# Performance work log

Measured on AMD Instinct MI355X. Metric: run time of the kernel, lower is better.

Reference implementation:

```python
import jax, jax.numpy as jnp
import numpy as np


def setup_inputs() -> dict:
    key = jax.random.key(0)
    ks = jax.random.split(key, 12)
    B, C, H, W = 8, 256, 64, 64
    C8 = C // 8
    s = lambda *sh: 0.02
    inp = {
        "x1": jax.random.normal(ks[0], (B, C, H, W), jnp.float32),
        "x2": jax.random.normal(ks[1], (B, C, H, W), jnp.float32),
        # DFEM.conv1 (1x1), shared for x1 and x2
        "w1": jax.random.normal(ks[2], (C, C), jnp.float32) * 0.02,
        "b1": jax.random.normal(ks[3], (C,), jnp.float32) * 0.02,
        # PAM projections (1x1 convs)
        "wq": jax.random.normal(ks[4], (C8, C), jnp.float32) * 0.02,
        "bq": jax.random.normal(ks[5], (C8,), jnp.float32) * 0.02,
        "wk": jax.random.normal(ks[6], (C8, C), jnp.float32) * 0.02,
        "bk": jax.random.normal(ks[7], (C8,), jnp.float32) * 0.02,
        "wv": jax.random.normal(ks[8], (C, C), jnp.float32) * 0.02,
        "bv": jax.random.normal(ks[9], (C,), jnp.float32) * 0.02,
        # gamma initialized to zero in the original; use small nonzero so PAM path matters
        "gamma": jnp.full((1,), 0.5, jnp.float32),
        # SpatialAttention 3x3 conv, 2->1 channels, no bias (OIHW)
        "w_sa": jax.random.normal(ks[10], (1, 2, 3, 3), jnp.float32) * 0.1,
    }
    return inp


def _conv1x1(x, w, b):
    # x: [B,C,H,W], w: [O,C], b: [O]
    return jnp.einsum("oc,bchw->bohw", w, x) + b[None, :, None, None]


def _pam(x, wq, bq, wk, bk, wv, bv, gamma):
    B, C, H, W = x.shape
    N = H * W
    xf = x.reshape(B, C, N)
    q = jnp.einsum("oc,bcn->bon", wq, xf) + bq[None, :, None]  # [B,C/8,N]
    k = jnp.einsum("oc,bcn->bon", wk, xf) + bk[None, :, None]  # [B,C/8,N]
    v = jnp.einsum("oc,bcn->bon", wv, xf) + bv[None, :, None]  # [B,C,N]
    energy = jnp.einsum("bci,bcj->bij", q, k)                  # [B,N,N] (no scaling, as in source)
    att = jax.nn.softmax(energy, axis=-1)
    out = jnp.einsum("bcj,bij->bci", v, att).reshape(B, C, H, W)
    return gamma[0] * out + x


def _spatial_attention(x, w_sa):
    # x: [B,2C,H,W] -> [B,1,H,W]
    avg_out = jnp.mean(x, axis=1, keepdims=True)
    max_out = jnp.max(x, axis=1, keepdims=True)
    cat = jnp.concatenate([avg_out, max_out], axis=1)  # [B,2,H,W]
    y = jax.lax.conv_general_dilated(
        cat, w_sa, window_strides=(1, 1), padding=((1, 1), (1, 1)),
        dimension_numbers=("NCHW", "OIHW", "NCHW"))
    return jax.nn.sigmoid(y)


def reference(x1, x2, w1, b1, wq, bq, wk, bk, wv, bv, gamma, w_sa):
    x11 = _conv1x1(x1, w1, b1)
    x21 = _conv1x1(x2, w1, b1)
    weight = _spatial_attention(jnp.concatenate([x11, x21], axis=1), w_sa)
    out1 = _pam(x11, wq, bq, wk, bk, wv, bv, gamma)
    out2 = _pam(x21, wq, bq, wk, bk, wv, bv, gamma)
    a = x1 * out1
    b = x2 * out2
    return weight * jnp.abs(b - a)
```

## Files before the change

### kernel.cpp

```cpp
#include <hip/hip_runtime.h>
#include <stdint.h>

#define B_ 8
#define C_ 256
#define N_ 4096
#define C8_ 32
#define LOG2E 1.4426950408889634f

typedef __attribute__((ext_vector_type(8))) short s16x8;
typedef __attribute__((ext_vector_type(4))) float f32x4;

static __device__ __forceinline__ unsigned short f2bf(float f) {
  union { float f; unsigned u; } v; v.f = f;
  unsigned r = v.u + 0x7FFFu + ((v.u >> 16) & 1u);
  return (unsigned short)(r >> 16);
}
static __device__ __forceinline__ float bf2f(unsigned short h) {
  union { unsigned u; float f; } v; v.u = ((unsigned)h) << 16;
  return v.f;
}
static __device__ __forceinline__ unsigned cvtpk(float lo, float hi) {
  unsigned r;
  asm("v_cvt_pk_bf16_f32 %0, %1, %2" : "=v"(r) : "v"(lo), "v"(hi));
  return r;
}

#define OFS_X1T  0ull
#define OFS_X2T  16777216ull
#define OFS_X11T 33554432ull
#define OFS_X21T 50331648ull
#define OFS_Q1   67108864ull
#define OFS_K1   69206016ull
#define OFS_Q2   71303168ull
#define OFS_K2   73400320ull
#define OFS_V1   75497472ull
#define OFS_V2   92274688ull
#define OFS_OA1  OFS_X1T
#define OFS_OA2  OFS_X2T
#define OFS_MM   109051904ull
#define OFS_WGT  109314048ull
#define OFS_W1B  109445120ull
#define OFS_WQB  109576192ull
#define OFS_WKB  109592576ull
#define OFS_WVB  109608960ull

__global__ __launch_bounds__(256) void k_transpose(
    const float* __restrict__ x1, const float* __restrict__ x2,
    unsigned short* __restrict__ x1t, unsigned short* __restrict__ x2t) {
  __shared__ unsigned short lds[64 * 66];
  const int t = threadIdx.x;
  const int b = blockIdx.z >> 1, s = blockIdx.z & 1;
  const float* src = s ? x2 : x1;
  unsigned short* dst = s ? x2t : x1t;
  const int n0 = blockIdx.x * 64, c0 = blockIdx.y * 64;
  const int nl = t & 63;
#pragma unroll
  for (int r = 0; r < 16; ++r) {
    const int cl = (t >> 6) + 4 * r;
    lds[nl * 66 + cl] = f2bf(src[((size_t)(b * C_ + c0 + cl)) * N_ + n0 + nl]);
  }
  __syncthreads();
  const int c2 = t & 31;
#pragma unroll
  for (int r = 0; r < 8; ++r) {
    const int n = (t >> 5) + 8 * r;
    const unsigned uv = *(const unsigned*)(&lds[n * 66 + 2 * c2]);
    *(unsigned*)(&dst[((size_t)(b * N_ + n0 + n)) * C_ + c0 + 2 * c2]) = uv;
  }
}

__global__ __launch_bounds__(256) void k_wconv(
    const float* __restrict__ w1, const float* __restrict__ wq,
    const float* __restrict__ wk, const float* __restrict__ wv,
    unsigned short* __restrict__ w1b, unsigned short* __restrict__ wqb,
    unsigned short* __restrict__ wkb, unsigned short* __restrict__ wvb) {
  const int i = blockIdx.x * 256 + threadIdx.x;
  if (i < 65536) { w1b[i] = f2bf(w1[i]); wvb[i] = f2bf(wv[i]); }
  if (i < 8192)  { wqb[i] = f2bf(wq[i]); wkb[i] = f2bf(wk[i]); }
}

__global__ __launch_bounds__(256) void k_conv(
    const unsigned short* __restrict__ X1, const unsigned short* __restrict__ X2,
    const unsigned short* __restrict__ W, const float* __restrict__ bias,
    unsigned short* __restrict__ O1, unsigned short* __restrict__ O2) {
  const unsigned short* X = blockIdx.z ? X2 : X1;
  unsigned short* OUT = blockIdx.z ? O2 : O1;
  const int b = blockIdx.y;
  const int lane = threadIdx.x & 63, wave = threadIdx.x >> 6;
  const int li = lane & 15, g = lane >> 4;
  const int nbase = blockIdx.x * 64 + wave * 16;
  const f32x4 zero4 = {0.f, 0.f, 0.f, 0.f};
  f32x4 acc[16];
#pragma unroll
  for (int f = 0; f < 16; ++f) acc[f] = zero4;
  const unsigned short* xrow = X + ((size_t)b * N_ + nbase + li) * C_ + 8 * g;
#pragma unroll
  for (int kk = 0; kk < 8; ++kk) {
    const s16x8 a = *(const s16x8*)(xrow + kk * 32);
#pragma unroll
    for (int f = 0; f < 16; ++f) {
      const s16x8 wf = *(const s16x8*)(W + ((size_t)(f * 16 + li)) * C_ + kk * 32 + 8 * g);
      acc[f] = __builtin_amdgcn_mfma_f32_16x16x32_bf16(wf, a, acc[f], 0, 0, 0);
    }
  }
  unsigned short* orow = OUT + ((size_t)b * N_ + nbase + li) * C_ + 4 * g;
#pragma unroll
  for (int f = 0; f < 16; ++f) {
    const float4 bb = *(const float4*)(bias + f * 16 + 4 * g);
    const unsigned lo = cvtpk(acc[f][0] + bb.x, acc[f][1] + bb.y);
    const unsigned hi = cvtpk(acc[f][2] + bb.z, acc[f][3] + bb.w);
    *(uint2*)(orow + f * 16) = make_uint2(lo, hi);
  }
}

__global__ __launch_bounds__(256) void k_qk(
    const unsigned short* __restrict__ X1, const unsigned short* __restrict__ X2,
    const unsigned short* __restrict__ WQ, const unsigned short* __restrict__ WK,
    const float* __restrict__ bq, const float* __restrict__ bk,
    unsigned short* __restrict__ Q1o, unsigned short* __restrict__ Q2o,
    unsigned short* __restrict__ K1o, unsigned short* __restrict__ K2o) {
  const unsigned short* X = blockIdx.z ? X2 : X1;
  unsigned short* Qo = blockIdx.z ? Q2o : Q1o;
  unsigned short* Ko = blockIdx.z ? K2o : K1o;
  const int b = blockIdx.y;
  const int lane = threadIdx.x & 63, wave = threadIdx.x >> 6;
  const int li = lane & 15, g = lane >> 4;
  const int nbase = blockIdx.x * 64 + wave * 16;
  const f32x4 zero4 = {0.f, 0.f, 0.f, 0.f};
  f32x4 aq[2], ak[2];
#pragma unroll
  for (int f = 0; f < 2; ++f) { aq[f] = zero4; ak[f] = zero4; }
  const unsigned short* xrow = X + ((size_t)b * N_ + nbase + li) * C_ + 8 * g;
#pragma unroll
  for (int kk = 0; kk < 8; ++kk) {
    const s16x8 a = *(const s16x8*)(xrow + kk * 32);
#pragma unroll
    for (int f = 0; f < 2; ++f) {
      const s16x8 wqf = *(const s16x8*)(WQ + ((size_t)(f * 16 + li)) * C_ + kk * 32 + 8 * g);
      const s16x8 wkf = *(const s16x8*)(WK + ((size_t)(f * 16 + li)) * C_ + kk * 32 + 8 * g);
      aq[f] = __builtin_amdgcn_mfma_f32_16x16x32_bf16(wqf, a, aq[f], 0, 0, 0);
      ak[f] = __builtin_amdgcn_mfma_f32_16x16x32_bf16(wkf, a, ak[f], 0, 0, 0);
    }
  }
  unsigned short* qrow = Qo + ((size_t)b * N_ + nbase + li) * C8_ + 4 * g;
  unsigned short* krow = Ko + ((size_t)b * N_ + nbase + li) * C8_ + 4 * g;
#pragma unroll
  for (int f = 0; f < 2; ++f) {
    const float4 bbq = *(const float4*)(bq + f * 16 + 4 * g);
    const float4 bbk = *(const float4*)(bk + f * 16 + 4 * g);
    const unsigned qlo = cvtpk((aq[f][0] + bbq.x) * LOG2E, (aq[f][1] + bbq.y) * LOG2E);
    const unsigned qhi = cvtpk((aq[f][2] + bbq.z) * LOG2E, (aq[f][3] + bbq.w) * LOG2E);
    const unsigned klo = cvtpk(ak[f][0] + bbk.x, ak[f][1] + bbk.y);
    const unsigned khi = cvtpk(ak[f][2] + bbk.z, ak[f][3] + bbk.w);
    *(uint2*)(qrow + f * 16) = make_uint2(qlo, qhi);
    *(uint2*)(krow + f * 16) = make_uint2(klo, khi);
  }
}

__global__ __launch_bounds__(256) void k_gemm_v(
    const unsigned short* __restrict__ X1, const unsigned short* __restrict__ X2,
    const unsigned short* __restrict__ W, const float* __restrict__ bias,
    unsigned short* __restrict__ V1o, unsigned short* __restrict__ V2o) {
  const int b = blockIdx.z >> 1, s = blockIdx.z & 1;
  const unsigned short* X = s ? X2 : X1;
  unsigned short* OUT = s ? V2o : V1o;
  const int lane = threadIdx.x & 63, wave = threadIdx.x >> 6;
  const int li = lane & 15, g = lane >> 4;
  const int obase = blockIdx.x * 64 + wave * 16;
  const int nbase = blockIdx.y * 256;
  const f32x4 zero4 = {0.f, 0.f, 0.f, 0.f};
  f32x4 acc[16];
#pragma unroll
  for (int f = 0; f < 16; ++f) acc[f] = zero4;
  const unsigned short* wrow = W + ((size_t)(obase + li)) * C_ + 8 * g;
#pragma unroll
  for (int kk = 0; kk < 8; ++kk) {
    const s16x8 a = *(const s16x8*)(wrow + kk * 32);
#pragma unroll
    for (int fn = 0; fn < 16; ++fn) {
      const s16x8 xf = *(const s16x8*)(X + ((size_t)b * N_ + nbase + fn * 16 + li) * C_ + kk * 32 + 8 * g);
      acc[fn] = __builtin_amdgcn_mfma_f32_16x16x32_bf16(xf, a, acc[fn], 0, 0, 0);
    }
  }
  const float bb = bias[obase + li];
  unsigned short* orow = OUT + ((size_t)b * C_ + obase + li) * N_ + nbase + 4 * g;
#pragma unroll
  for (int fn = 0; fn < 16; ++fn) {
    const unsigned lo = cvtpk(acc[fn][0] + bb, acc[fn][1] + bb);
    const unsigned hi = cvtpk(acc[fn][2] + bb, acc[fn][3] + bb);
    *(uint2*)(orow + fn * 16) = make_uint2(lo, hi);
  }
}

__global__ __launch_bounds__(256, 2) void k_flash2(
    const unsigned short* __restrict__ Q1, const unsigned short* __restrict__ K1,
    const unsigned short* __restrict__ V1, unsigned short* __restrict__ OA1,
    const unsigned short* __restrict__ Q2, const unsigned short* __restrict__ K2,
    const unsigned short* __restrict__ V2, unsigned short* __restrict__ OA2) {
  __shared__ __attribute__((aligned(16))) unsigned short vtile[2][8192];
  __shared__ __attribute__((aligned(16))) unsigned short ptile[4][1024];
  const int t = threadIdx.x;
  int f = blockIdx.x;
  f = (f & 7) * 64 + (f >> 3);
  const int z = f >> 5, qt = f & 31;
  const int b = z >> 1, src = z & 1;
  const unsigned short* Qp = src ? Q2 : Q1;
  const unsigned short* Kp = src ? K2 : K1;
  const unsigned short* Vp = src ? V2 : V1;
  unsigned short* OAp = (src ? OA2 : OA1) + (size_t)b * C_ * N_;

  const int lane = t & 63, wave = t >> 6;
  const int li = lane & 15, g = lane >> 4;
  const int rsw = (li >> 1) & 3;
  const f32x4 zero4 = {0.f, 0.f, 0.f, 0.f};

  const unsigned short* Vb = Vp + (size_t)b * C_ * N_;
  const unsigned short* Kb = Kp + (size_t)b * N_ * C8_;
  const int qbase = qt * 128 + wave * 32;

  s16x8 qf[2];
#pragma unroll
  for (int ib = 0; ib < 2; ++ib)
    qf[ib] = *(const s16x8*)(Qp + ((size_t)b * N_ + qbase + ib * 16 + li) * C8_ + 8 * g);

  f32x4 acc[2][16];
#pragma unroll
  for (int ib = 0; ib < 2; ++ib)
#pragma unroll
    for (int fc = 0; fc < 16; ++fc) acc[ib][fc] = zero4;
  float lsum[2] = {0.f, 0.f};

  const int vrow0 = t >> 2, vJ = t & 3;
  const int vwoff = ((vJ ^ ((vrow0 >> 1) & 3)) << 4);
  const int prd = ((g ^ rsw) << 4);
  const int psw0 = (((g >> 1) ^ rsw) << 4) + (g & 1) * 8;
  const int psw1 = ((((g >> 1) | 2) ^ rsw) << 4) + (g & 1) * 8;
  char* const pb = (char*)ptile[wave];

  int4 vreg[4];
#pragma unroll
  for (int rep = 0; rep < 4; ++rep)
    vreg[rep] = *(const int4*)(Vb + (size_t)(vrow0 + rep * 64) * N_ + vJ * 8);
  s16x8 kf0, kf1;
  {
    const unsigned short* kp = Kb + (size_t)li * C8_ + 8 * g;
    kf0 = *(const s16x8*)kp;
    kf1 = *(const s16x8*)(kp + 16 * C8_);
  }
#pragma unroll
  for (int rep = 0; rep < 4; ++rep)
    *(int4*)((char*)vtile[0] + (vrow0 + rep * 64) * 64 + vwoff) = vreg[rep];
  __syncthreads();

  for (int jt = 0; jt < 128; ++jt) {
    const int cur = jt & 1;
    const int jbn = ((jt + 1) & 127) * 32;
#pragma unroll
    for (int rep = 0; rep < 4; ++rep)
      vreg[rep] = *(const int4*)(Vb + (size_t)(vrow0 + rep * 64) * N_ + jbn + vJ * 8);
    s16x8 kn0, kn1;
    {
      const unsigned short* kp = Kb + (size_t)(jbn + li) * C8_ + 8 * g;
      kn0 = *(const s16x8*)kp;
      kn1 = *(const s16x8*)(kp + 16 * C8_);
    }

#pragma unroll
    for (int ib = 0; ib < 2; ++ib) {
      const f32x4 s0 = __builtin_amdgcn_mfma_f32_16x16x32_bf16(kf0, qf[ib], zero4, 0, 0, 0);
      const f32x4 s1 = __builtin_amdgcn_mfma_f32_16x16x32_bf16(kf1, qf[ib], zero4, 0, 0, 0);
      const float p0 = exp2f(s0[0] - 8.f), p1 = exp2f(s0[1] - 8.f);
      const float p2 = exp2f(s0[2] - 8.f), p3 = exp2f(s0[3] - 8.f);
      const float p4 = exp2f(s1[0] - 8.f), p5 = exp2f(s1[1] - 8.f);
      const float p6 = exp2f(s1[2] - 8.f), p7 = exp2f(s1[3] - 8.f);
      lsum[ib] += ((p0 + p1) + (p2 + p3)) + ((p4 + p5) + (p6 + p7));
      const unsigned u01 = cvtpk(p0, p1), u23 = cvtpk(p2, p3);
      const unsigned u45 = cvtpk(p4, p5), u67 = cvtpk(p6, p7);
      char* const pr = pb + (ib * 16 + li) * 64;
      *(uint2*)(pr + psw0) = make_uint2(u01, u23);
      *(uint2*)(pr + psw1) = make_uint2(u45, u67);
    }

    const s16x8 pb0 = *(const s16x8*)(pb + li * 64 + prd);
    const s16x8 pb1 = *(const s16x8*)(pb + (16 + li) * 64 + prd);
    char* const vt = (char*)vtile[cur];
#pragma unroll
    for (int fc = 0; fc < 16; ++fc) {
      const s16x8 vf = *(const s16x8*)(vt + (fc * 16 + li) * 64 + prd);
      acc[0][fc] = __builtin_amdgcn_mfma_f32_16x16x32_bf16(vf, pb0, acc[0][fc], 0, 0, 0);
      acc[1][fc] = __builtin_amdgcn_mfma_f32_16x16x32_bf16(vf, pb1, acc[1][fc], 0, 0, 0);
    }

#pragma unroll
    for (int rep = 0; rep < 4; ++rep)
      *(int4*)((char*)vtile[cur ^ 1] + (vrow0 + rep * 64) * 64 + vwoff) = vreg[rep];
    kf0 = kn0; kf1 = kn1;
    __syncthreads();
  }

#pragma unroll
  for (int ib = 0; ib < 2; ++ib) {
    float ls = lsum[ib];
    ls += __shfl_xor(ls, 16);
    ls += __shfl_xor(ls, 32);
    const float inv = 1.0f / ls;
    unsigned short* oab = OAp + qbase + ib * 16 + li;
#pragma unroll
    for (int fc = 0; fc < 16; ++fc) {
#pragma unroll
      for (int r = 0; r < 4; ++r) {
        oab[(size_t)(fc * 16 + 4 * g + r) * N_] = f2bf(acc[ib][fc][r] * inv);
      }
    }
  }
}

__global__ __launch_bounds__(256) void k_sared(
    const unsigned short* __restrict__ x11t, const unsigned short* __restrict__ x21t,
    float* __restrict__ mm) {
  const int row = blockIdx.x * 4 + (threadIdx.x >> 6);
  const int lane = threadIdx.x & 63;
  float s = 0.f, mx = -1e30f;
  const uint2 a = *(const uint2*)(x11t + (size_t)row * C_ + lane * 4);
  const uint2 c = *(const uint2*)(x21t + (size_t)row * C_ + lane * 4);
  const unsigned vals[4] = {a.x, a.y, c.x, c.y};
#pragma unroll
  for (int k = 0; k < 4; ++k) {
    const float f0 = bf2f((unsigned short)(vals[k] & 0xffff));
    const float f1 = bf2f((unsigned short)(vals[k] >> 16));
    s += f0 + f1;
    mx = fmaxf(mx, fmaxf(f0, f1));
  }
#pragma unroll
  for (int off = 1; off < 64; off <<= 1) {
    s += __shfl_xor(s, off);
    mx = fmaxf(mx, __shfl_xor(mx, off));
  }
  if (lane == 0) {
    const int b = row >> 12, n = row & 4095;
    mm[(size_t)b * 8192 + n] = s * (1.f / 512.f);
    mm[(size_t)b * 8192 + 4096 + n] = mx;
  }
}

__global__ __launch_bounds__(256) void k_saconv(
    const float* __restrict__ mm, const float* __restrict__ wsa, float* __restrict__ wgt) {
  const int gi = blockIdx.x * 256 + threadIdx.x;
  const int b = gi >> 12, n = gi & 4095, h = n >> 6, w = n & 63;
  float acc = 0.f;
#pragma unroll
  for (int ky = 0; ky < 3; ++ky) {
#pragma unroll
    for (int kx = 0; kx < 3; ++kx) {
      const int hh = h + ky - 1, ww = w + kx - 1;
      if (hh >= 0 && hh < 64 && ww >= 0 && ww < 64) {
        const int nn = hh * 64 + ww;
        acc += mm[(size_t)b * 8192 + nn] * wsa[ky * 3 + kx];
        acc += mm[(size_t)b * 8192 + 4096 + nn] * wsa[9 + ky * 3 + kx];
      }
    }
  }
  wgt[gi] = 1.f / (1.f + __expf(-acc));
}

__global__ __launch_bounds__(256) void k_final(
    const float* __restrict__ x1, const float* __restrict__ x2,
    const unsigned short* __restrict__ x11t, const unsigned short* __restrict__ x21t,
    const unsigned short* __restrict__ oa1, const unsigned short* __restrict__ oa2,
    const float* __restrict__ wgt, const float* __restrict__ gamma,
    float* __restrict__ out) {
  __shared__ unsigned short t1[64 * 66], t2[64 * 66];
  const int t = threadIdx.x;
  const int b = blockIdx.z, c0 = blockIdx.y * 64, n0 = blockIdx.x * 64;
#pragma unroll
  for (int r = 0; r < 16; ++r) {
    const int nl = (t >> 6) + 4 * r, cl = t & 63;
    const size_t idx = ((size_t)b * N_ + n0 + nl) * C_ + c0 + cl;
    t1[nl * 66 + cl] = x11t[idx];
    t2[nl * 66 + cl] = x21t[idx];
  }
  __syncthreads();
  const float gam = gamma[0];
#pragma unroll
  for (int r = 0; r < 16; ++r) {
    const int cl = (t >> 6) + 4 * r, nl = t & 63;
    const size_t idx = ((size_t)b * C_ + c0 + cl) * N_ + n0 + nl;
    const float o1 = gam * bf2f(oa1[idx]) + bf2f(t1[nl * 66 + cl]);
    const float o2 = gam * bf2f(oa2[idx]) + bf2f(t2[nl * 66 + cl]);
    const float av = x1[idx] * o1;
    const float bv = x2[idx] * o2;
    out[idx] = wgt[(size_t)b * N_ + n0 + nl] * fabsf(bv - av);
  }
}

extern "C" void kernel_launch(void* const* d_in, const int* in_sizes, int n_in,
                              void* d_out, int out_size, void* d_ws, size_t ws_size,
                              hipStream_t stream) {
  const float* x1 = (const float*)d_in[0];
  const float* x2 = (const float*)d_in[1];
  const float* w1 = (const float*)d_in[2];
  const float* b1 = (const float*)d_in[3];
  const float* wq = (const float*)d_in[4];
  const float* bq = (const float*)d_in[5];
  const float* wk = (const float*)d_in[6];
  const float* bk = (const float*)d_in[7];
  const float* wv = (const float*)d_in[8];
  const float* bv = (const float*)d_in[9];
  const float* gamma = (const float*)d_in[10];
  const float* wsa = (const float*)d_in[11];
  float* out = (float*)d_out;
  char* ws = (char*)d_ws;

  unsigned short* x1T  = (unsigned short*)(ws + OFS_X1T);
  unsigned short* x2T  = (unsigned short*)(ws + OFS_X2T);
  unsigned short* x11T = (unsigned short*)(ws + OFS_X11T);
  unsigned short* x21T = (unsigned short*)(ws + OFS_X21T);
  unsigned short* Q1   = (unsigned short*)(ws + OFS_Q1);
  unsigned short* K1   = (unsigned short*)(ws + OFS_K1);
  unsigned short* Q2   = (unsigned short*)(ws + OFS_Q2);
  unsigned short* K2   = (unsigned short*)(ws + OFS_K2);
  unsigned short* V1   = (unsigned short*)(ws + OFS_V1);
  unsigned short* V2   = (unsigned short*)(ws + OFS_V2);
  unsigned short* oa1  = (unsigned short*)(ws + OFS_OA1);
  unsigned short* oa2  = (unsigned short*)(ws + OFS_OA2);
  float* mm  = (float*)(ws + OFS_MM);
  float* wgt = (float*)(ws + OFS_WGT);
  unsigned short* w1b = (unsigned short*)(ws + OFS_W1B);
  unsigned short* wqb = (unsigned short*)(ws + OFS_WQB);
  unsigned short* wkb = (unsigned short*)(ws + OFS_WKB);
  unsigned short* wvb = (unsigned short*)(ws + OFS_WVB);

  k_transpose<<<dim3(64, 4, 16), 256, 0, stream>>>(x1, x2, x1T, x2T);
  k_wconv<<<256, 256, 0, stream>>>(w1, wq, wk, wv, w1b, wqb, wkb, wvb);

  k_conv<<<dim3(64, 8, 2), 256, 0, stream>>>(x1T, x2T, w1b, b1, x11T, x21T);
  k_qk<<<dim3(64, 8, 2), 256, 0, stream>>>(x11T, x21T, wqb, wkb, bq, bk, Q1, Q2, K1, K2);
  k_gemm_v<<<dim3(4, 16, 16), 256, 0, stream>>>(x11T, x21T, wvb, bv, V1, V2);

  k_sared<<<8192, 256, 0, stream>>>(x11T, x21T, mm);
  k_saconv<<<128, 256, 0, stream>>>(mm, wsa, wgt);

  k_flash2<<<512, 256, 0, stream>>>(Q1, K1, V1, oa1, Q2, K2, V2, oa2);

  k_final<<<dim3(64, 4, 8), 256, 0, stream>>>(x1, x2, x11T, x21T, oa1, oa2, wgt, gamma, out);
}
```

Before: 574.6 us.

## Load V fragments straight from global memory in flash kernel, dropping LDS staging

The attention kernel no longer stages V tiles through double-buffered shared memory with a block-wide barrier each iteration. Each wave now loads its MFMA V operands directly from global memory into registers, software-pipelined in groups of four across the unrolled PV MFMAs, and the per-tile __syncthreads goes away. Intent is to cut LDS traffic and barrier stalls and free shared memory. In exchange every wave re-reads V from global/L2 (four waves per block duplicate those loads), and the register pressure could hurt occupancy now that the min-blocks launch bound is removed.

```diff
diff --git a/kernel.cpp b/kernel.cpp
--- a/kernel.cpp
+++ b/kernel.cpp
@@ -192,12 +192,11 @@
   }
 }
 
-__global__ __launch_bounds__(256, 2) void k_flash2(
+__global__ __launch_bounds__(256) void k_flash3(
     const unsigned short* __restrict__ Q1, const unsigned short* __restrict__ K1,
     const unsigned short* __restrict__ V1, unsigned short* __restrict__ OA1,
     const unsigned short* __restrict__ Q2, const unsigned short* __restrict__ K2,
     const unsigned short* __restrict__ V2, unsigned short* __restrict__ OA2) {
-  __shared__ __attribute__((aligned(16))) unsigned short vtile[2][8192];
   __shared__ __attribute__((aligned(16))) unsigned short ptile[4][1024];
   const int t = threadIdx.x;
   int f = blockIdx.x;
@@ -214,7 +213,7 @@
   const int rsw = (li >> 1) & 3;
   const f32x4 zero4 = {0.f, 0.f, 0.f, 0.f};
 
-  const unsigned short* Vb = Vp + (size_t)b * C_ * N_;
+  const unsigned short* Vb = Vp + (size_t)b * C_ * N_ + (size_t)li * N_ + 8 * g;
   const unsigned short* Kb = Kp + (size_t)b * N_ * C8_;
   const int qbase = qt * 128 + wave * 32;
 
@@ -230,34 +229,31 @@
     for (int fc = 0; fc < 16; ++fc) acc[ib][fc] = zero4;
   float lsum[2] = {0.f, 0.f};
 
-  const int vrow0 = t >> 2, vJ = t & 3;
-  const int vwoff = ((vJ ^ ((vrow0 >> 1) & 3)) << 4);
   const int prd = ((g ^ rsw) << 4);
   const int psw0 = (((g >> 1) ^ rsw) << 4) + (g & 1) * 8;
   const int psw1 = ((((g >> 1) | 2) ^ rsw) << 4) + (g & 1) * 8;
   char* const pb = (char*)ptile[wave];
 
-  int4 vreg[4];
-#pragma unroll
-  for (int rep = 0; rep < 4; ++rep)
-    vreg[rep] = *(const int4*)(Vb + (size_t)(vrow0 + rep * 64) * N_ + vJ * 8);
+#define VLD(fc, jb) (*(const s16x8*)(Vb + (size_t)((fc) * 16) * N_ + (jb)))
+
   s16x8 kf0, kf1;
   {
     const unsigned short* kp = Kb + (size_t)li * C8_ + 8 * g;
     kf0 = *(const s16x8*)kp;
     kf1 = *(const s16x8*)(kp + 16 * C8_);
   }
-#pragma unroll
-  for (int rep = 0; rep < 4; ++rep)
-    *(int4*)((char*)vtile[0] + (vrow0 + rep * 64) * 64 + vwoff) = vreg[rep];
-  __syncthreads();
+  s16x8 vA0 = VLD(0, 0), vA1 = VLD(1, 0), vA2 = VLD(2, 0), vA3 = VLD(3, 0);
 
   for (int jt = 0; jt < 128; ++jt) {
-    const int cur = jt & 1;
+    const int jb = jt * 32;
     const int jbn = ((jt + 1) & 127) * 32;
-#pragma unroll
-    for (int rep = 0; rep < 4; ++rep)
-      vreg[rep] = *(const int4*)(Vb + (size_t)(vrow0 + rep * 64) * N_ + jbn + vJ * 8);
+
+    const f32x4 s0a = __builtin_amdgcn_mfma_f32_16x16x32_bf16(kf0, qf[0], zero4, 0, 0, 0);
+    const f32x4 s1a = __builtin_amdgcn_mfma_f32_16x16x32_bf16(kf1, qf[0], zero4, 0, 0, 0);
+    const f32x4 s0b = __builtin_amdgcn_mfma_f32_16x16x32_bf16(kf0, qf[1], zero4, 0, 0, 0);
+    const f32x4 s1b = __builtin_amdgcn_mfma_f32_16x16x32_bf16(kf1, qf[1], zero4, 0, 0, 0);
+
+    s16x8 vB0 = VLD(4, jb), vB1 = VLD(5, jb), vB2 = VLD(6, jb), vB3 = VLD(7, jb);
     s16x8 kn0, kn1;
     {
       const unsigned short* kp = Kb + (size_t)(jbn + li) * C8_ + 8 * g;
@@ -265,38 +261,68 @@
       kn1 = *(const s16x8*)(kp + 16 * C8_);
     }
 
-#pragma unroll
-    for (int ib = 0; ib < 2; ++ib) {
-      const f32x4 s0 = __builtin_amdgcn_mfma_f32_16x16x32_bf16(kf0, qf[ib], zero4, 0, 0, 0);
-      const f32x4 s1 = __builtin_amdgcn_mfma_f32_16x16x32_bf16(kf1, qf[ib], zero4, 0, 0, 0);
-      const float p0 = exp2f(s0[0] - 8.f), p1 = exp2f(s0[1] - 8.f);
-      const float p2 = exp2f(s0[2] - 8.f), p3 = exp2f(s0[3] - 8.f);
-      const float p4 = exp2f(s1[0] - 8.f), p5 = exp2f(s1[1] - 8.f);
-      const float p6 = exp2f(s1[2] - 8.f), p7 = exp2f(s1[3] - 8.f);
-      lsum[ib] += ((p0 + p1) + (p2 + p3)) + ((p4 + p5) + (p6 + p7));
-      const unsigned u01 = cvtpk(p0, p1), u23 = cvtpk(p2, p3);
-      const unsigned u45 = cvtpk(p4, p5), u67 = cvtpk(p6, p7);
-      char* const pr = pb + (ib * 16 + li) * 64;
-      *(uint2*)(pr + psw0) = make_uint2(u01, u23);
-      *(uint2*)(pr + psw1) = make_uint2(u45, u67);
-    }
-
+    {
+      const float p0 = exp2f(s0a[0] - 8.f), p1 = exp2f(s0a[1] - 8.f);
+      const float p2 = exp2f(s0a[2] - 8.f), p3 = exp2f(s0a[3] - 8.f);
+      const float p4 = exp2f(s1a[0] - 8.f), p5 = exp2f(s1a[1] - 8.f);
+      const float p6 = exp2f(s1a[2] - 8.f), p7 = exp2f(s1a[3] - 8.f);
+      lsum[0] += ((p0 + p1) + (p2 + p3)) + ((p4 + p5) + (p6 + p7));
+      char* const pr = pb + li * 64;
+      *(uint2*)(pr + psw0) = make_uint2(cvtpk(p0, p1), cvtpk(p2, p3));
+      *(uint2*)(pr + psw1) = make_uint2(cvtpk(p4, p5), cvtpk(p6, p7));
+    }
+    {
+      const float p0 = exp2f(s0b[0] - 8.f), p1 = exp2f(s0b[1] - 8.f);
+      const float p2 = exp2f(s0b[2] - 8.f), p3 = exp2f(s0b[3] - 8.f);
+      const float p4 = exp2f(s1b[0] - 8.f), p5 = exp2f(s1b[1] - 8.f);
+      const float p6 = exp2f(s1b[2] - 8.f), p7 = exp2f(s1b[3] - 8.f);
+      lsum[1] += ((p0 + p1) + (p2 + p3)) + ((p4 + p5) + (p6 + p7));
+      char* const pr = pb + (16 + li) * 64;
+      *(uint2*)(pr + psw0) = make_uint2(cvtpk(p0, p1), cvtpk(p2, p3));
+      *(uint2*)(pr + psw1) = make_uint2(cvtpk(p4, p5), cvtpk(p6, p7));
+    }
     const s16x8 pb0 = *(const s16x8*)(pb + li * 64 + prd);
     const s16x8 pb1 = *(const s16x8*)(pb + (16 + li) * 64 + prd);
-    char* const vt = (char*)vtile[cur];
-#pragma unroll
-    for (int fc = 0; fc < 16; ++fc) {
-      const s16x8 vf = *(const s16x8*)(vt + (fc * 16 + li) * 64 + prd);
-      acc[0][fc] = __builtin_amdgcn_mfma_f32_16x16x32_bf16(vf, pb0, acc[0][fc], 0, 0, 0);
-      acc[1][fc] = __builtin_amdgcn_mfma_f32_16x16x32_bf16(vf, pb1, acc[1][fc], 0, 0, 0);
-    }
-
-#pragma unroll
-    for (int rep = 0; rep < 4; ++rep)
-      *(int4*)((char*)vtile[cur ^ 1] + (vrow0 + rep * 64) * 64 + vwoff) = vreg[rep];
+
+    acc[0][0] = __builtin_amdgcn_mfma_f32_16x16x32_bf16(vA0, pb0, acc[0][0], 0, 0, 0);
+    acc[1][0] = __builtin_amdgcn_mfma_f32_16x16x32_bf16(vA0, pb1, acc[1][0], 0, 0, 0);
+    acc[0][1] = __builtin_amdgcn_mfma_f32_16x16x32_bf16(vA1, pb0, acc[0][1], 0, 0, 0);
+    acc[1][1] = __builtin_amdgcn_mfma_f32_16x16x32_bf16(vA1, pb1, acc[1][1], 0, 0, 0);
+    acc[0][2] = __builtin_amdgcn_mfma_f32_16x16x32_bf16(vA2, pb0, acc[0][2], 0, 0, 0);
+    acc[1][2] = __builtin_amdgcn_mfma_f32_16x16x32_bf16(vA2, pb1, acc[1][2], 0, 0, 0);
+    acc[0][3] = __builtin_amdgcn_mfma_f32_16x16x32_bf16(vA3, pb0, acc[0][3], 0, 0, 0);
+    acc[1][3] = __builtin_amdgcn_mfma_f32_16x16x32_bf16(vA3, pb1, acc[1][3], 0, 0, 0);
+    vA0 = VLD(8, jb); vA1 = VLD(9, jb); vA2 = VLD(10, jb); vA3 = VLD(11, jb);
+    acc[0][4] = __builtin_amdgcn_mfma_f32_16x16x32_bf16(vB0, pb0, acc[0][4], 0, 0, 0);
+    acc[1][4] = __builtin_amdgcn_mfma_f32_16x16x32_bf16(vB0, pb1, acc[1][4], 0, 0, 0);
+    acc[0][5] = __builtin_amdgcn_mfma_f32_16x16x32_bf16(vB1, pb0, acc[0][5], 0, 0, 0);
+    acc[1][5] = __builtin_amdgcn_mfma_f32_16x16x32_bf16(vB1, pb1, acc[1][5], 0, 0, 0);
+    acc[0][6] = __builtin_amdgcn_mfma_f32_16x16x32_bf16(vB2, pb0, acc[0][6], 0, 0, 0);
+    acc[1][6] = __builtin_amdgcn_mfma_f32_16x16x32_bf16(vB2, pb1, acc[1][6], 0, 0, 0);
+    acc[0][7] = __builtin_amdgcn_mfma_f32_16x16x32_bf16(vB3, pb0, acc[0][7], 0, 0, 0);
+    acc[1][7] = __builtin_amdgcn_mfma_f32_16x16x32_bf16(vB3, pb1, acc[1][7], 0, 0, 0);
+    vB0 = VLD(12, jb); vB1 = VLD(13, jb); vB2 = VLD(14, jb); vB3 = VLD(15, jb);
+    acc[0][8] = __builtin_amdgcn_mfma_f32_16x16x32_bf16(vA0, pb0, acc[0][8], 0, 0, 0);
+    acc[1][8] = __builtin_amdgcn_mfma_f32_16x16x32_bf16(vA0, pb1, acc[1][8], 0, 0, 0);
+    acc[0][9] = __builtin_amdgcn_mfma_f32_16x16x32_bf16(vA1, pb0, acc[0][9], 0, 0, 0);
+    acc[1][9] = __builtin_amdgcn_mfma_f32_16x16x32_bf16(vA1, pb1, acc[1][9], 0, 0, 0);
+    acc[0][10] = __builtin_amdgcn_mfma_f32_16x16x32_bf16(vA2, pb0, acc[0][10], 0, 0, 0);
+    acc[1][10] = __builtin_amdgcn_mfma_f32_16x16x32_bf16(vA2, pb1, acc[1][10], 0, 0, 0);
+    acc[0][11] = __builtin_amdgcn_mfma_f32_16x16x32_bf16(vA3, pb0, acc[0][11], 0, 0, 0);
+    acc[1][11] = __builtin_amdgcn_mfma_f32_16x16x32_bf16(vA3, pb1, acc[1][11], 0, 0, 0);
+    vA0 = VLD(0, jbn); vA1 = VLD(1, jbn); vA2 = VLD(2, jbn); vA3 = VLD(3, jbn);
+    acc[0][12] = __builtin_amdgcn_mfma_f32_16x16x32_bf16(vB0, pb0, acc[0][12], 0, 0, 0);
+    acc[1][12] = __builtin_amdgcn_mfma_f32_16x16x32_bf16(vB0, pb1, acc[1][12], 0, 0, 0);
+    acc[0][13] = __builtin_amdgcn_mfma_f32_16x16x32_bf16(vB1, pb0, acc[0][13], 0, 0, 0);
+    acc[1][13] = __builtin_amdgcn_mfma_f32_16x16x32_bf16(vB1, pb1, acc[1][13], 0, 0, 0);
+    acc[0][14] = __builtin_amdgcn_mfma_f32_16x16x32_bf16(vB2, pb0, acc[0][14], 0, 0, 0);
+    acc[1][14] = __builtin_amdgcn_mfma_f32_16x16x32_bf16(vB2, pb1, acc[1][14], 0, 0, 0);
+    acc[0][15] = __builtin_amdgcn_mfma_f32_16x16x32_bf16(vB3, pb0, acc[0][15], 0, 0, 0);
+    acc[1][15] = __builtin_amdgcn_mfma_f32_16x16x32_bf16(vB3, pb1, acc[1][15], 0, 0, 0);
+
     kf0 = kn0; kf1 = kn1;
-    __syncthreads();
-  }
+  }
+#undef VLD
 
 #pragma unroll
   for (int ib = 0; ib < 2; ++ib) {
@@ -440,7 +466,7 @@
   k_sared<<<8192, 256, 0, stream>>>(x11T, x21T, mm);
   k_saconv<<<128, 256, 0, stream>>>(mm, wsa, wgt);
 
-  k_flash2<<<512, 256, 0, stream>>>(Q1, K1, V1, oa1, Q2, K2, V2, oa2);
+  k_flash3<<<512, 256, 0, stream>>>(Q1, K1, V1, oa1, Q2, K2, V2, oa2);
 
   k_final<<<dim3(64, 4, 8), 256, 0, stream>>>(x1, x2, x11T, x21T, oa1, oa2, wgt, gamma, out);
 }
```

New measurement: 832.9 us. 1.45x slower.

## Split attention KV range across two workgroups with separate normalization pass

Applied to the files above, without the earlier changes.

Splits the key/value loop of the flash attention kernel into two halves processed by separate workgroups. Each half writes unnormalized partial outputs and row sums, and a new k_norm kernel sums them and normalizes. The path is enabled only when the workspace is large enough. Also raises wave priority around the MFMA loop. This aims to improve CU utilization and latency hiding at the cost of extra partial-output memory traffic and a kernel launch.

```diff
diff --git a/kernel.cpp b/kernel.cpp
--- a/kernel.cpp
+++ b/kernel.cpp
@@ -35,14 +35,16 @@
 #define OFS_K2   73400320ull
 #define OFS_V1   75497472ull
 #define OFS_V2   92274688ull
-#define OFS_OA1  OFS_X1T
-#define OFS_OA2  OFS_X2T
 #define OFS_MM   109051904ull
 #define OFS_WGT  109314048ull
 #define OFS_W1B  109445120ull
 #define OFS_WQB  109576192ull
 #define OFS_WKB  109592576ull
 #define OFS_WVB  109608960ull
+#define OFS_LS   109740032ull
+#define OFS_P2H0 117440512ull
+#define OFS_P2H1 134217728ull
+#define WS_NEED_SPLIT 150994944ull
 
 __global__ __launch_bounds__(256) void k_transpose(
     const float* __restrict__ x1, const float* __restrict__ x2,
@@ -192,22 +194,32 @@
   }
 }
 
-__global__ __launch_bounds__(256, 2) void k_flash2(
+__global__ __launch_bounds__(256, 2) void k_flash2s(
     const unsigned short* __restrict__ Q1, const unsigned short* __restrict__ K1,
-    const unsigned short* __restrict__ V1, unsigned short* __restrict__ OA1,
+    const unsigned short* __restrict__ V1,
     const unsigned short* __restrict__ Q2, const unsigned short* __restrict__ K2,
-    const unsigned short* __restrict__ V2, unsigned short* __restrict__ OA2) {
+    const unsigned short* __restrict__ V2,
+    unsigned short* __restrict__ P1h0, unsigned short* __restrict__ P1h1,
+    unsigned short* __restrict__ P2h0, unsigned short* __restrict__ P2h1,
+    float* __restrict__ LS, int nh) {
   __shared__ __attribute__((aligned(16))) unsigned short vtile[2][8192];
   __shared__ __attribute__((aligned(16))) unsigned short ptile[4][1024];
   const int t = threadIdx.x;
+  const int lg2nh = nh >> 1;
   int f = blockIdx.x;
-  f = (f & 7) * 64 + (f >> 3);
-  const int z = f >> 5, qt = f & 31;
+  const int nwg8 = (512 * nh) >> 3;
+  f = (f & 7) * nwg8 + (f >> 3);
+  const int h = f & (nh - 1);
+  const int rest = f >> lg2nh;
+  const int z = rest >> 5, qt = rest & 31;
   const int b = z >> 1, src = z & 1;
+  const int jts = 128 >> lg2nh;
+  const int jof = h * jts;
+
   const unsigned short* Qp = src ? Q2 : Q1;
   const unsigned short* Kp = src ? K2 : K1;
   const unsigned short* Vp = src ? V2 : V1;
-  unsigned short* OAp = (src ? OA2 : OA1) + (size_t)b * C_ * N_;
+  unsigned short* OAp = (src ? (h ? P2h1 : P2h0) : (h ? P1h1 : P1h0)) + (size_t)b * C_ * N_;
 
   const int lane = t & 63, wave = t >> 6;
   const int li = lane & 15, g = lane >> 4;
@@ -240,10 +252,10 @@
   int4 vreg[4];
 #pragma unroll
   for (int rep = 0; rep < 4; ++rep)
-    vreg[rep] = *(const int4*)(Vb + (size_t)(vrow0 + rep * 64) * N_ + vJ * 8);
+    vreg[rep] = *(const int4*)(Vb + (size_t)(vrow0 + rep * 64) * N_ + jof * 32 + vJ * 8);
   s16x8 kf0, kf1;
   {
-    const unsigned short* kp = Kb + (size_t)li * C8_ + 8 * g;
+    const unsigned short* kp = Kb + (size_t)(jof * 32 + li) * C8_ + 8 * g;
     kf0 = *(const s16x8*)kp;
     kf1 = *(const s16x8*)(kp + 16 * C8_);
   }
@@ -252,9 +264,9 @@
     *(int4*)((char*)vtile[0] + (vrow0 + rep * 64) * 64 + vwoff) = vreg[rep];
   __syncthreads();
 
-  for (int jt = 0; jt < 128; ++jt) {
-    const int cur = jt & 1;
-    const int jbn = ((jt + 1) & 127) * 32;
+  for (int lt = 0; lt < jts; ++lt) {
+    const int cur = lt & 1;
+    const int jbn = (jof + ((lt + 1) & (jts - 1))) * 32;
 #pragma unroll
     for (int rep = 0; rep < 4; ++rep)
       vreg[rep] = *(const int4*)(Vb + (size_t)(vrow0 + rep * 64) * N_ + jbn + vJ * 8);
@@ -284,12 +296,14 @@
     const s16x8 pb0 = *(const s16x8*)(pb + li * 64 + prd);
     const s16x8 pb1 = *(const s16x8*)(pb + (16 + li) * 64 + prd);
     char* const vt = (char*)vtile[cur];
+    __builtin_amdgcn_s_setprio(1);
 #pragma unroll
     for (int fc = 0; fc < 16; ++fc) {
       const s16x8 vf = *(const s16x8*)(vt + (fc * 16 + li) * 64 + prd);
       acc[0][fc] = __builtin_amdgcn_mfma_f32_16x16x32_bf16(vf, pb0, acc[0][fc], 0, 0, 0);
       acc[1][fc] = __builtin_amdgcn_mfma_f32_16x16x32_bf16(vf, pb1, acc[1][fc], 0, 0, 0);
     }
+    __builtin_amdgcn_s_setprio(0);
 
 #pragma unroll
     for (int rep = 0; rep < 4; ++rep)
@@ -303,7 +317,9 @@
     float ls = lsum[ib];
     ls += __shfl_xor(ls, 16);
     ls += __shfl_xor(ls, 32);
-    const float inv = 1.0f / ls;
+    if (g == 0)
+      LS[(size_t)((src * 2 + h) * 8 + b) * N_ + qbase + ib * 16 + li] = ls;
+    const float inv = (nh == 2) ? 1.0f : 1.0f / ls;
     unsigned short* oab = OAp + qbase + ib * 16 + li;
 #pragma unroll
     for (int fc = 0; fc < 16; ++fc) {
@@ -313,6 +329,42 @@
       }
     }
   }
+}
+
+__global__ __launch_bounds__(256) void k_norm(
+    unsigned short* __restrict__ P1h0, const unsigned short* __restrict__ P1h1,
+    unsigned short* __restrict__ P2h0, const unsigned short* __restrict__ P2h1,
+    const float* __restrict__ LS) {
+  const int e = blockIdx.x * 256 + threadIdx.x;
+  const int n0 = (e & 511) * 8;
+  const int c = (e >> 9) & 255;
+  const int b = (e >> 17) & 7;
+  const int s = e >> 20;
+  unsigned short* pA = (s ? P2h0 : P1h0) + ((size_t)(b * C_ + c)) * N_ + n0;
+  const unsigned short* pBp = (s ? P2h1 : P1h1) + ((size_t)(b * C_ + c)) * N_ + n0;
+  const float* lA = LS + (size_t)((s * 2 + 0) * 8 + b) * N_ + n0;
+  const float* lB = LS + (size_t)((s * 2 + 1) * 8 + b) * N_ + n0;
+  const uint4 a = *(const uint4*)pA;
+  const uint4 bb = *(const uint4*)pBp;
+  const float4 la0 = *(const float4*)lA, la1 = *(const float4*)(lA + 4);
+  const float4 lb0 = *(const float4*)lB, lb1 = *(const float4*)(lB + 4);
+  const unsigned av[4] = {a.x, a.y, a.z, a.w};
+  const unsigned bv[4] = {bb.x, bb.y, bb.z, bb.w};
+  const float il[8] = {
+      1.f / (la0.x + lb0.x), 1.f / (la0.y + lb0.y),
+      1.f / (la0.z + lb0.z), 1.f / (la0.w + lb0.w),
+      1.f / (la1.x + lb1.x), 1.f / (la1.y + lb1.y),
+      1.f / (la1.z + lb1.z), 1.f / (la1.w + lb1.w)};
+  unsigned out[4];
+#pragma unroll
+  for (int k = 0; k < 4; ++k) {
+    const float o0 = (bf2f((unsigned short)(av[k] & 0xffff)) +
+                      bf2f((unsigned short)(bv[k] & 0xffff))) * il[2 * k];
+    const float o1 = (bf2f((unsigned short)(av[k] >> 16)) +
+                      bf2f((unsigned short)(bv[k] >> 16))) * il[2 * k + 1];
+    out[k] = cvtpk(o0, o1);
+  }
+  *(uint4*)pA = make_uint4(out[0], out[1], out[2], out[3]);
 }
 
 __global__ __launch_bounds__(256) void k_sared(
@@ -421,14 +473,24 @@
   unsigned short* K2   = (unsigned short*)(ws + OFS_K2);
   unsigned short* V1   = (unsigned short*)(ws + OFS_V1);
   unsigned short* V2   = (unsigned short*)(ws + OFS_V2);
-  unsigned short* oa1  = (unsigned short*)(ws + OFS_OA1);
-  unsigned short* oa2  = (unsigned short*)(ws + OFS_OA2);
   float* mm  = (float*)(ws + OFS_MM);
   float* wgt = (float*)(ws + OFS_WGT);
   unsigned short* w1b = (unsigned short*)(ws + OFS_W1B);
   unsigned short* wqb = (unsigned short*)(ws + OFS_WQB);
   unsigned short* wkb = (unsigned short*)(ws + OFS_WKB);
   unsigned short* wvb = (unsigned short*)(ws + OFS_WVB);
+  float* LS = (float*)(ws + OFS_LS);
+
+  const bool split = (ws_size >= WS_NEED_SPLIT);
+  const int nh = split ? 2 : 1;
+  unsigned short* P1h0 = (unsigned short*)(ws + OFS_X1T);
+  unsigned short* P1h1 = (unsigned short*)(ws + OFS_X2T);
+  unsigned short* P2h0 = split ? (unsigned short*)(ws + OFS_P2H0)
+                               : (unsigned short*)(ws + OFS_X2T);
+  unsigned short* P2h1 = split ? (unsigned short*)(ws + OFS_P2H1)
+                               : (unsigned short*)(ws + OFS_X2T);
+  unsigned short* oa1 = P1h0;
+  unsigned short* oa2 = P2h0;
 
   k_transpose<<<dim3(64, 4, 16), 256, 0, stream>>>(x1, x2, x1T, x2T);
   k_wconv<<<256, 256, 0, stream>>>(w1, wq, wk, wv, w1b, wqb, wkb, wvb);
@@ -440,7 +502,11 @@
   k_sared<<<8192, 256, 0, stream>>>(x11T, x21T, mm);
   k_saconv<<<128, 256, 0, stream>>>(mm, wsa, wgt);
 
-  k_flash2<<<512, 256, 0, stream>>>(Q1, K1, V1, oa1, Q2, K2, V2, oa2);
+  k_flash2s<<<512 * nh, 256, 0, stream>>>(Q1, K1, V1, Q2, K2, V2,
+                                          P1h0, P1h1, P2h0, P2h1, LS, nh);
+  if (split) {
+    k_norm<<<8192, 256, 0, stream>>>(P1h0, P1h1, P2h0, P2h1, LS);
+  }
 
   k_final<<<dim3(64, 4, 8), 256, 0, stream>>>(x1, x2, x11T, x21T, oa1, oa2, wgt, gamma, out);
 }
```

Result: slower. 687.7 us (+19.7%).
